# Optimization experiments

Hardware: AMD Instinct MI355X
Metric: run time of the kernel (lower is better)

## Reference

```python
import jax, jax.numpy as jnp
import numpy as np

B, S, D, DQK, DV = 4, 2048, 1024, 128, 256
EPS = 1e-8


def setup_inputs() -> dict:
    key = jax.random.key(0)
    ks = jax.random.split(key, 11)
    s = lambda fan_in: 1.0 / np.sqrt(fan_in)
    return {
        "X": jax.random.normal(ks[0], (B, S, D), dtype=jnp.float32),
        "Wq": jax.random.uniform(ks[1], (D, DQK), minval=-s(D), maxval=s(D), dtype=jnp.float32),
        "bq": jax.random.uniform(ks[2], (DQK,), minval=-s(D), maxval=s(D), dtype=jnp.float32),
        "Wk": jax.random.uniform(ks[3], (D, DQK), minval=-s(D), maxval=s(D), dtype=jnp.float32),
        "bk": jax.random.uniform(ks[4], (DQK,), minval=-s(D), maxval=s(D), dtype=jnp.float32),
        "Wv": jax.random.uniform(ks[5], (D, DV), minval=-s(D), maxval=s(D), dtype=jnp.float32),
        "bv": jax.random.uniform(ks[6], (DV,), minval=-s(D), maxval=s(D), dtype=jnp.float32),
        "Wg": jax.random.uniform(ks[7], (D, DV), minval=-s(D), maxval=s(D), dtype=jnp.float32),
        "bg": jax.random.uniform(ks[8], (DV,), minval=-s(D), maxval=s(D), dtype=jnp.float32),
        "Wp": jax.random.uniform(ks[9], (DV, D), minval=-s(DV), maxval=s(DV), dtype=jnp.float32),
        "bp": jax.random.uniform(ks[10], (D,), minval=-s(DV), maxval=s(DV), dtype=jnp.float32),
    }


def _shepards(Q, K, V, p=2, eps=EPS):
    # Euclidean cdist via ||q||^2 + ||k||^2 - 2 q.k  (then sqrt)
    q2 = jnp.sum(Q * Q, axis=-1, keepdims=True)          # [B,Sq,1]
    k2 = jnp.sum(K * K, axis=-1, keepdims=True)          # [B,Sk,1]
    d2 = q2 + jnp.swapaxes(k2, -1, -2) - 2.0 * jnp.einsum("bqd,bkd->bqk", Q, K)
    Dm = jnp.sqrt(jnp.maximum(d2, 0.0))                  # [B,Sq,Sk]
    W = jnp.power(jnp.maximum(Dm, eps), -float(p))
    A = W / jnp.sum(W, axis=2, keepdims=True)
    return jnp.einsum("bqk,bkv->bqv", A, V)


def reference(X, Wq, bq, Wk, bk, Wv, bv, Wg, bg, Wp, bp):
    N = X  # norm is Identity
    Q = N @ Wq + bq
    K = N @ Wk + bk
    V = N @ Wv + bv
    A = _shepards(Q, K, V)
    G = N @ Wg + bg
    return X + (A * G) @ Wp + bp
```

## Files before the change

### kernel.cpp

```cpp
#include <hip/hip_runtime.h>
#include <stdint.h>

#define SLEN 2048
#define NROWS 8192

typedef __attribute__((ext_vector_type(4))) float f32x4;
typedef __attribute__((ext_vector_type(8))) short bf16x8;
typedef __attribute__((ext_vector_type(2))) unsigned int u32x2;
typedef __attribute__((ext_vector_type(4))) unsigned int u32x4;

__device__ __forceinline__ short f2bf(float f) {
  uint32_t u = __builtin_bit_cast(uint32_t, f);
  u += 0x7FFFu + ((u >> 16) & 1u);
  return (short)(u >> 16);
}
__device__ __forceinline__ float bf2f(short s) {
  uint32_t u = ((uint32_t)(uint16_t)s) << 16;
  return __builtin_bit_cast(float, u);
}
__device__ __forceinline__ f32x4 mfma16(bf16x8 a, bf16x8 b, f32x4 c) {
  return __builtin_amdgcn_mfma_f32_16x16x32_bf16(a, b, c, 0, 0, 0);
}
__device__ __forceinline__ void gld_lds16(const void* g, void* l) {
  __builtin_amdgcn_global_load_lds(
      (const __attribute__((address_space(1))) void*)g,
      (__attribute__((address_space(3))) void*)l, 16, 0, 0);
}

__global__ __launch_bounds__(256) void k_prep(
    const float* __restrict__ Wq, const float* __restrict__ bq,
    const float* __restrict__ Wk, const float* __restrict__ bk,
    const float* __restrict__ Wv, const float* __restrict__ bv,
    const float* __restrict__ Wg, const float* __restrict__ bg,
    const float* __restrict__ Wp,
    short* __restrict__ WcatT, short* __restrict__ WpT,
    float* __restrict__ bcat) {
  __shared__ short tl[64][72];
  int blk = blockIdx.x, tid = threadIdx.x;
  if (blk < 256) {
    int t = blk;
    const float* src; short* dst; int C, rowoff, dstC, r0, c0;
    if (t < 32)       { src = Wq; C = 128;  rowoff = 0;   dst = WcatT; dstC = 1024; r0 = (t >> 1) * 64;  c0 = (t & 1) * 64; }
    else if (t < 64)  { t -= 32;  src = Wk; C = 128;  rowoff = 128; dst = WcatT; dstC = 1024; r0 = (t >> 1) * 64;  c0 = (t & 1) * 64; }
    else if (t < 128) { t -= 64;  src = Wv; C = 256;  rowoff = 256; dst = WcatT; dstC = 1024; r0 = (t >> 2) * 64;  c0 = (t & 3) * 64; }
    else if (t < 192) { t -= 128; src = Wg; C = 256;  rowoff = 512; dst = WcatT; dstC = 1024; r0 = (t >> 2) * 64;  c0 = (t & 3) * 64; }
    else              { t -= 192; src = Wp; C = 1024; rowoff = 0;   dst = WpT;   dstC = 256;  r0 = (t >> 4) * 64;  c0 = (t & 15) * 64; }
    int lr = tid >> 4, lcc = tid & 15;
#pragma unroll
    for (int rr = 0; rr < 4; ++rr) {
      f32x4 v = *(const f32x4*)&src[(size_t)(r0 + lr * 4 + rr) * C + c0 + lcc * 4];
#pragma unroll
      for (int j = 0; j < 4; ++j) tl[lcc * 4 + j][lr * 4 + rr] = f2bf(v[j]);
    }
    __syncthreads();
    int orow = tid >> 2, og = (tid & 3) * 16;
    bf16x8 o1, o2;
#pragma unroll
    for (int j = 0; j < 8; ++j) { o1[j] = tl[orow][og + j]; o2[j] = tl[orow][og + 8 + j]; }
    size_t dbase = (size_t)(rowoff + c0 + orow) * dstC + r0 + og;
    *(bf16x8*)&dst[dbase] = o1;
    *(bf16x8*)&dst[dbase + 8] = o2;
  } else {
    int c = tid;
    if (c < 768) {
      float v;
      if (c < 128)      v = bq[c];
      else if (c < 256) v = bk[c - 128];
      else if (c < 512) v = bv[c - 256];
      else              v = bg[c - 512];
      bcat[c] = v;
    }
  }
}

__global__ __launch_bounds__(256) void k_gemm1(
    const float* __restrict__ X, const short* __restrict__ WcatT,
    const float* __restrict__ bcat, short* __restrict__ O,
    float* __restrict__ q2a, float* __restrict__ k2a) {
  __shared__ float Atf[128 * 32];
  __shared__ short Bt[128 * 32];
  __shared__ float nlds[128][2];
  const int tid = threadIdx.x;
  const int w = tid >> 6, l = tid & 63, lg = l >> 4, lc = l & 15;
  const int m0 = blockIdx.x * 128, n0 = blockIdx.y * 128;
  const int sr0 = w * 32 + (l >> 2);
  const int scc = (l & 3) * 8;
  const int wm = (w >> 1) * 64, wn = (w & 1) * 64;
  const int arow = w * 8 + (l >> 3);
  const int achk = (l & 7) ^ (arow & 7);

  f32x4 acc[4][4] = {};
  const float* Ab = X + (size_t)m0 * 1024;
  const short* Bb = WcatT + (size_t)n0 * 1024;

  for (int kb = 0; kb < 1024; kb += 32) {
#pragma unroll
    for (int i = 0; i < 4; ++i)
      gld_lds16(Ab + (size_t)(i * 32 + arow) * 1024 + kb + achk * 4,
                &Atf[(i * 32 + w * 8) * 32 + l * 4]);
    gld_lds16(Bb + (size_t)sr0 * 1024 + kb + scc, &Bt[(w * 32) * 32]);
    gld_lds16(Bb + (size_t)(sr0 + 16) * 1024 + kb + scc, &Bt[(w * 32 + 16) * 32]);
    __syncthreads();
    bf16x8 af[4], bf[4];
#pragma unroll
    for (int mi = 0; mi < 4; ++mi) {
      int r = wm + mi * 16 + lc;
      f32x4 a0 = *(const f32x4*)&Atf[r * 32 + (((2 * lg) ^ (r & 7)) * 4)];
      f32x4 a1 = *(const f32x4*)&Atf[r * 32 + (((2 * lg + 1) ^ (r & 7)) * 4)];
#pragma unroll
      for (int j = 0; j < 4; ++j) {
        af[mi][j] = f2bf(a0[j]);
        af[mi][4 + j] = f2bf(a1[j]);
      }
    }
#pragma unroll
    for (int ni = 0; ni < 4; ++ni)
      bf[ni] = *(const bf16x8*)&Bt[(wn + ni * 16 + lc) * 32 + lg * 8];
#pragma unroll
    for (int mi = 0; mi < 4; ++mi)
#pragma unroll
      for (int ni = 0; ni < 4; ++ni)
        acc[mi][ni] = mfma16(af[mi], bf[ni], acc[mi][ni]);
    __syncthreads();
  }
  float sq[4][4] = {};
#pragma unroll
  for (int mi = 0; mi < 4; ++mi) {
    int gr = m0 + wm + mi * 16 + lg * 4;
#pragma unroll
    for (int ni = 0; ni < 4; ++ni) {
      int gc = n0 + wn + ni * 16 + lc;
      float bias = bcat[gc];
#pragma unroll
      for (int r = 0; r < 4; ++r) {
        short sv = f2bf(acc[mi][ni][r] + bias);
        O[(size_t)(gr + r) * 768 + gc] = sv;
        float v = bf2f(sv);
        sq[mi][r] += v * v;
      }
    }
  }
  if (blockIdx.y < 2) {
#pragma unroll
    for (int mi = 0; mi < 4; ++mi)
#pragma unroll
      for (int r = 0; r < 4; ++r) {
        float v = sq[mi][r];
        v += __shfl_xor(v, 1, 64); v += __shfl_xor(v, 2, 64);
        v += __shfl_xor(v, 4, 64); v += __shfl_xor(v, 8, 64);
        sq[mi][r] = v;
      }
    if (lc == 0) {
#pragma unroll
      for (int mi = 0; mi < 4; ++mi)
#pragma unroll
        for (int r = 0; r < 4; ++r)
          nlds[wm + mi * 16 + lg * 4 + r][w & 1] = sq[mi][r];
    }
    __syncthreads();
    if (tid < 128) {
      float t = nlds[tid][0] + nlds[tid][1];
      (blockIdx.y == 0 ? q2a : k2a)[m0 + tid] = t;
    }
  }
}

__global__ __launch_bounds__(256) void k_vt(
    const short* __restrict__ O, short* __restrict__ Vtp) {
  __shared__ short tile[64][33];
  int blk = blockIdx.x, tid = threadIdx.x;
  int b = blk >> 8, rem = blk & 255;
  int s0 = (rem >> 3) * 64, dv0 = (rem & 7) * 32;
  int r = tid >> 2, cg = (tid & 3) * 8;
  bf16x8 v = *(const bf16x8*)&O[(size_t)(b * SLEN + s0 + r) * 768 + 256 + dv0 + cg];
#pragma unroll
  for (int j = 0; j < 8; ++j) tile[r][cg + j] = v[j];
  __syncthreads();
  int dr = tid >> 3, sg = (tid & 7) * 8;
  bf16x8 ov;
#pragma unroll
  for (int j = 0; j < 8; ++j) ov[j] = tile[sg + j][dr];
  int ka = s0 + sg;
  int c5 = ka >> 5, hi = (ka >> 4) & 1, lgq = (ka >> 2) & 3;
  size_t base = (size_t)(b * 256 + dv0 + dr) * SLEN + c5 * 32 + lgq * 8 + hi * 4;
  u32x4 od = __builtin_bit_cast(u32x4, ov);
  u32x2 p0; p0[0] = od[0]; p0[1] = od[1];
  u32x2 p1; p1[0] = od[2]; p1[1] = od[3];
  *(u32x2*)&Vtp[base] = p0;
  *(u32x2*)&Vtp[base + 8] = p1;
}

__global__ __launch_bounds__(512) void k_attn(
    const short* __restrict__ O, const short* __restrict__ Vtp,
    const float* __restrict__ q2a, const float* __restrict__ k2a,
    short* __restrict__ nump, float* __restrict__ denp) {
  __shared__ short Klds[2][64 * 128];
  __shared__ short Vlds[2][256 * 64];
  const int tid = threadIdx.x;
  const int w = tid >> 6, l = tid & 63, lg = l >> 4, lc = l & 15;
  const int gid = blockIdx.x;
  const int blk = ((gid & 7) << 5) | (gid >> 3);
  const int b = blk >> 6, qt = (blk >> 2) & 15, ks = blk & 3;
  const int grow0 = b * SLEN + qt * 128 + w * 16;
  const int kbase = ks * 512;

  bf16x8 qf[4];
#pragma unroll
  for (int kf = 0; kf < 4; ++kf)
    qf[kf] = *(const bf16x8*)&O[(size_t)(grow0 + lc) * 768 + kf * 32 + lg * 8];
  const float q2s = q2a[grow0 + lc];

  f32x4 acc[16] = {};
  float den = 0.f;

#define STAGE(T, BSEL)                                                        \
  {                                                                           \
    const int kt_ = kbase + (T) * 64;                                         \
    _Pragma("unroll")                                                         \
    for (int j = 0; j < 6; ++j) {                                             \
      int issue = w * 6 + j;                                                  \
      if (issue < 16) {                                                       \
        int kk = issue * 4 + (l >> 4);                                        \
        int c = l & 15;                                                       \
        const short* src = O + (size_t)(b * SLEN + kt_ + kk) * 768 + 128 +    \
                           ((c ^ (kk & 7)) * 8);                              \
        gld_lds16(src, &Klds[BSEL][issue * 512 + l * 8]);                     \
      } else {                                                                \
        int vj = issue - 16;                                                  \
        int dv = vj * 8 + (l >> 3);                                           \
        int c = l & 7;                                                        \
        const short* src = Vtp + (size_t)(b * 256 + dv) * SLEN + kt_ +        \
                           ((c ^ (dv & 7)) * 8);                              \
        gld_lds16(src, &Vlds[BSEL][vj * 512 + l * 8]);                        \
      }                                                                       \
    }                                                                         \
  }

  STAGE(0, 0);
  for (int t = 0; t < 8; ++t) {
    __syncthreads();
    if (t < 7) STAGE(t + 1, (t + 1) & 1);
    const int bsel = t & 1;
    const int kb = b * SLEN + kbase + t * 64;
    f32x4 s[4] = {};
#pragma unroll
    for (int e = 0; e < 4; ++e)
#pragma unroll
      for (int kf = 0; kf < 4; ++kf) {
        bf16x8 kv = *(const bf16x8*)&Klds[bsel][(e * 16 + lc) * 128 +
                                               (((kf * 4 + lg) ^ (lc & 7)) * 8)];
        s[e] = mfma16(kv, qf[kf], s[e]);
      }
    float wv[4][4];
#pragma unroll
    for (int e = 0; e < 4; ++e) {
      f32x4 k2v = *(const f32x4*)&k2a[kb + e * 16 + lg * 4];
#pragma unroll
      for (int r = 0; r < 4; ++r) {
        float d2 = q2s + k2v[r] - 2.0f * s[e][r];
        float g = __builtin_amdgcn_rcpf(fmaxf(d2, 1e-16f));
        wv[e][r] = g;
        den += g;
      }
    }
#pragma unroll
    for (int ksub = 0; ksub < 2; ++ksub) {
      bf16x8 pa;
#pragma unroll
      for (int r = 0; r < 4; ++r) {
        pa[r] = f2bf(wv[2 * ksub][r]);
        pa[4 + r] = f2bf(wv[2 * ksub + 1][r]);
      }
#pragma unroll
      for (int nv = 0; nv < 16; ++nv) {
        int dv = nv * 16 + lc;
        bf16x8 bv = *(const bf16x8*)&Vlds[bsel][dv * 64 +
                                               (((ksub * 4 + lg) ^ (dv & 7)) * 8)];
        acc[nv] = mfma16(pa, bv, acc[nv]);
      }
    }
  }
#undef STAGE
  den += __shfl_xor(den, 16, 64);
  den += __shfl_xor(den, 32, 64);
  const int qt32 = qt * 4 + (w >> 1);
  const int pb = ((b * 64 + qt32) << 2) | ks;
  if (l < 16) denp[pb * 32 + (w & 1) * 16 + lc] = den;
  const size_t pbase = (size_t)pb * 32 * 256;
#pragma unroll
  for (int nv = 0; nv < 16; ++nv) {
    int dv = nv * 16 + lc;
#pragma unroll
    for (int r = 0; r < 4; ++r) {
      int rit = (w & 1) * 16 + lg * 4 + r;
      nump[pbase + (size_t)rit * 256 + dv] = f2bf(acc[nv][r]);
    }
  }
}

__global__ __launch_bounds__(256) void k_gemm3(
    const short* __restrict__ nump, const float* __restrict__ denp,
    const short* __restrict__ O, const short* __restrict__ WpT,
    const float* __restrict__ X, const float* __restrict__ bp,
    float* __restrict__ Y) {
  __shared__ short AGt[128 * 256];
  __shared__ short Bt[128 * 32];
  const int tid = threadIdx.x;
  const int w = tid >> 6, l = tid & 63, lg = l >> 4, lc = l & 15;
  const int bid = blockIdx.x;
  const int m0 = (bid & 63) * 128, n0 = (bid >> 6) * 128;
  const int sr0 = w * 32 + (l >> 2);
  const int scc = (l & 3) * 8;
  const int wm = (w >> 1) * 64, wn = (w & 1) * 64;

  {
    int r = tid >> 1;
    int row = m0 + r;
    int b_ = row >> 11, srow = row & 2047;
    int qt = srow >> 5, rit = srow & 31;
    int pbb = (b_ * 64 + qt) * 4;
    float den = 0.f;
#pragma unroll
    for (int ksi = 0; ksi < 4; ++ksi) den += denp[(pbb + ksi) * 32 + rit];
    float rden = 1.f / den;
    int dvh = (tid & 1) * 128;
#pragma unroll
    for (int ch = 0; ch < 16; ++ch) {
      int dv0 = dvh + ch * 8;
      float num[8] = {};
#pragma unroll
      for (int ksi = 0; ksi < 4; ++ksi) {
        bf16x8 v = *(const bf16x8*)&nump[((size_t)(pbb + ksi) * 32 + rit) * 256 + dv0];
#pragma unroll
        for (int j = 0; j < 8; ++j) num[j] += bf2f(v[j]);
      }
      bf16x8 gv = *(const bf16x8*)&O[(size_t)row * 768 + 512 + dv0];
      bf16x8 o;
#pragma unroll
      for (int j = 0; j < 8; ++j) o[j] = f2bf(num[j] * rden * bf2f(gv[j]));
      int byte = (r * 512 + dv0 * 2) ^ ((r & 31) << 4);
      *(bf16x8*)((char*)AGt + byte) = o;
    }
  }

  f32x4 acc[4][4] = {};
  const short* Bb = WpT + (size_t)n0 * 256;

  for (int kb = 0; kb < 256; kb += 32) {
    gld_lds16(Bb + (size_t)sr0 * 256 + kb + scc, &Bt[(w * 32) * 32]);
    gld_lds16(Bb + (size_t)(sr0 + 16) * 256 + kb + scc, &Bt[(w * 32 + 16) * 32]);
    __syncthreads();
    bf16x8 af[4], bf[4];
#pragma unroll
    for (int mi = 0; mi < 4; ++mi) {
      int r = wm + mi * 16 + lc;
      int byte = (r * 512 + (kb + lg * 8) * 2) ^ ((r & 31) << 4);
      af[mi] = *(const bf16x8*)((const char*)AGt + byte);
    }
#pragma unroll
    for (int ni = 0; ni < 4; ++ni)
      bf[ni] = *(const bf16x8*)&Bt[(wn + ni * 16 + lc) * 32 + lg * 8];
#pragma unroll
    for (int mi = 0; mi < 4; ++mi)
#pragma unroll
      for (int ni = 0; ni < 4; ++ni)
        acc[mi][ni] = mfma16(af[mi], bf[ni], acc[mi][ni]);
    __syncthreads();
  }
#pragma unroll
  for (int mi = 0; mi < 4; ++mi) {
    int gr = m0 + wm + mi * 16 + lg * 4;
#pragma unroll
    for (int ni = 0; ni < 4; ++ni) {
      int gc = n0 + wn + ni * 16 + lc;
      float bias = bp[gc];
#pragma unroll
      for (int r = 0; r < 4; ++r) {
        size_t idx = (size_t)(gr + r) * 1024 + gc;
        Y[idx] = acc[mi][ni][r] + X[idx] + bias;
      }
    }
  }
}

extern "C" void kernel_launch(void* const* d_in, const int* in_sizes, int n_in,
                              void* d_out, int out_size, void* d_ws, size_t ws_size,
                              hipStream_t stream) {
  const float* X  = (const float*)d_in[0];
  const float* Wq = (const float*)d_in[1];
  const float* bq = (const float*)d_in[2];
  const float* Wk = (const float*)d_in[3];
  const float* bk = (const float*)d_in[4];
  const float* Wv = (const float*)d_in[5];
  const float* bv = (const float*)d_in[6];
  const float* Wg = (const float*)d_in[7];
  const float* bg = (const float*)d_in[8];
  const float* Wp = (const float*)d_in[9];
  const float* bp = (const float*)d_in[10];

  char* ws = (char*)d_ws;
  short* WcatT = (short*)(ws + 0);
  short* WpT   = (short*)(ws + 1572864);
  float* bcat  = (float*)(ws + 2097152);
  short* O     = (short*)(ws + 2101248);
  short* Vtp   = (short*)(ws + 14684160);
  float* q2a   = (float*)(ws + 18878464);
  float* k2a   = (float*)(ws + 18911232);
  short* nump  = (short*)(ws + 18944000);
  float* denp  = (float*)(ws + 35721216);
  float* Y = (float*)d_out;

  hipLaunchKernelGGL(k_prep, dim3(257), dim3(256), 0, stream,
                     Wq, bq, Wk, bk, Wv, bv, Wg, bg, Wp, WcatT, WpT, bcat);
  hipLaunchKernelGGL(k_gemm1, dim3(64, 6), dim3(256), 0, stream, X, WcatT, bcat, O, q2a, k2a);
  hipLaunchKernelGGL(k_vt, dim3(1024), dim3(256), 0, stream, O, Vtp);
  hipLaunchKernelGGL(k_attn, dim3(256), dim3(512), 0, stream, O, Vtp, q2a, k2a, nump, denp);
  hipLaunchKernelGGL(k_gemm3, dim3(512), dim3(256), 0, stream, nump, denp, O, WpT, X, bp, Y);
}
```

Baseline: 216.8 us.

## Split split-K reduction and gating out of output GEMM into separate kernel

Moves the reduction of the partial numerators and denominators, the normalisation and the gate multiply out of k_gemm3 into a new elementwise kernel k_red that writes a bf16 AG buffer. k_gemm3 then becomes a plain tiled GEMM that streams both A and B through small LDS tiles instead of a 64KB LDS A panel. Before, each of the 8 column blocks redundantly recomputed the reduction for its rows. The aim is to remove that redundant work and raise occupancy, at the cost of one extra launch and an extra write and read of AG.

```diff
diff --git a/kernel.cpp b/kernel.cpp
--- a/kernel.cpp
+++ b/kernel.cpp
@@ -298,65 +298,61 @@
   }
 }
 
+__global__ __launch_bounds__(256) void k_red(
+    const short* __restrict__ nump, const float* __restrict__ denp,
+    const short* __restrict__ O, short* __restrict__ AG) {
+  int flat = blockIdx.x * 256 + threadIdx.x;
+  int idx8 = flat * 8;
+  int row = idx8 >> 8;
+  int dv0 = idx8 & 255;
+  int b = row >> 11, srow = row & 2047;
+  int qt = srow >> 5, rit = srow & 31;
+  int blkbase = (b * 64 + qt) << 2;
+  float num[8] = {};
+  float den = 0.f;
+#pragma unroll
+  for (int ksi = 0; ksi < 4; ++ksi) {
+    const size_t base = ((size_t)(blkbase + ksi) * 32 + rit) * 256 + dv0;
+    bf16x8 v = *(const bf16x8*)&nump[base];
+#pragma unroll
+    for (int j = 0; j < 8; ++j) num[j] += bf2f(v[j]);
+    den += denp[(blkbase + ksi) * 32 + rit];
+  }
+  float rden = 1.f / den;
+  bf16x8 gv = *(const bf16x8*)&O[(size_t)row * 768 + 512 + dv0];
+  bf16x8 o;
+#pragma unroll
+  for (int j = 0; j < 8; ++j) o[j] = f2bf(num[j] * rden * bf2f(gv[j]));
+  *(bf16x8*)&AG[idx8] = o;
+}
+
 __global__ __launch_bounds__(256) void k_gemm3(
-    const short* __restrict__ nump, const float* __restrict__ denp,
-    const short* __restrict__ O, const short* __restrict__ WpT,
+    const short* __restrict__ AG, const short* __restrict__ WpT,
     const float* __restrict__ X, const float* __restrict__ bp,
     float* __restrict__ Y) {
-  __shared__ short AGt[128 * 256];
+  __shared__ short At[128 * 32];
   __shared__ short Bt[128 * 32];
   const int tid = threadIdx.x;
   const int w = tid >> 6, l = tid & 63, lg = l >> 4, lc = l & 15;
-  const int bid = blockIdx.x;
-  const int m0 = (bid & 63) * 128, n0 = (bid >> 6) * 128;
+  const int m0 = blockIdx.x * 128, n0 = blockIdx.y * 128;
   const int sr0 = w * 32 + (l >> 2);
   const int scc = (l & 3) * 8;
   const int wm = (w >> 1) * 64, wn = (w & 1) * 64;
 
-  {
-    int r = tid >> 1;
-    int row = m0 + r;
-    int b_ = row >> 11, srow = row & 2047;
-    int qt = srow >> 5, rit = srow & 31;
-    int pbb = (b_ * 64 + qt) * 4;
-    float den = 0.f;
-#pragma unroll
-    for (int ksi = 0; ksi < 4; ++ksi) den += denp[(pbb + ksi) * 32 + rit];
-    float rden = 1.f / den;
-    int dvh = (tid & 1) * 128;
-#pragma unroll
-    for (int ch = 0; ch < 16; ++ch) {
-      int dv0 = dvh + ch * 8;
-      float num[8] = {};
-#pragma unroll
-      for (int ksi = 0; ksi < 4; ++ksi) {
-        bf16x8 v = *(const bf16x8*)&nump[((size_t)(pbb + ksi) * 32 + rit) * 256 + dv0];
-#pragma unroll
-        for (int j = 0; j < 8; ++j) num[j] += bf2f(v[j]);
-      }
-      bf16x8 gv = *(const bf16x8*)&O[(size_t)row * 768 + 512 + dv0];
-      bf16x8 o;
-#pragma unroll
-      for (int j = 0; j < 8; ++j) o[j] = f2bf(num[j] * rden * bf2f(gv[j]));
-      int byte = (r * 512 + dv0 * 2) ^ ((r & 31) << 4);
-      *(bf16x8*)((char*)AGt + byte) = o;
-    }
-  }
-
   f32x4 acc[4][4] = {};
+  const short* Ab = AG + (size_t)m0 * 256;
   const short* Bb = WpT + (size_t)n0 * 256;
 
   for (int kb = 0; kb < 256; kb += 32) {
+    gld_lds16(Ab + (size_t)sr0 * 256 + kb + scc, &At[(w * 32) * 32]);
+    gld_lds16(Ab + (size_t)(sr0 + 16) * 256 + kb + scc, &At[(w * 32 + 16) * 32]);
     gld_lds16(Bb + (size_t)sr0 * 256 + kb + scc, &Bt[(w * 32) * 32]);
     gld_lds16(Bb + (size_t)(sr0 + 16) * 256 + kb + scc, &Bt[(w * 32 + 16) * 32]);
     __syncthreads();
     bf16x8 af[4], bf[4];
 #pragma unroll
-    for (int mi = 0; mi < 4; ++mi) {
-      int r = wm + mi * 16 + lc;
-      int byte = (r * 512 + (kb + lg * 8) * 2) ^ ((r & 31) << 4);
-      af[mi] = *(const bf16x8*)((const char*)AGt + byte);
-    }
+    for (int mi = 0; mi < 4; ++mi)
+      af[mi] = *(const bf16x8*)&At[(wm + mi * 16 + lc) * 32 + lg * 8];
 #pragma unroll
     for (int ni = 0; ni < 4; ++ni)
       bf[ni] = *(const bf16x8*)&Bt[(wn + ni * 16 + lc) * 32 + lg * 8];
@@ -408,6 +404,7 @@
   float* k2a   = (float*)(ws + 18911232);
   short* nump  = (short*)(ws + 18944000);
   float* denp  = (float*)(ws + 35721216);
+  short* AG    = (short*)(ws + 35852288);
   float* Y = (float*)d_out;
 
   hipLaunchKernelGGL(k_prep, dim3(257), dim3(256), 0, stream,
@@ -415,5 +412,6 @@
   hipLaunchKernelGGL(k_gemm1, dim3(64, 6), dim3(256), 0, stream, X, WcatT, bcat, O, q2a, k2a);
   hipLaunchKernelGGL(k_vt, dim3(1024), dim3(256), 0, stream, O, Vtp);
   hipLaunchKernelGGL(k_attn, dim3(256), dim3(512), 0, stream, O, Vtp, q2a, k2a, nump, denp);
-  hipLaunchKernelGGL(k_gemm3, dim3(512), dim3(256), 0, stream, nump, denp, O, WpT, X, bp, Y);
-}
+  hipLaunchKernelGGL(k_red, dim3(1024), dim3(256), 0, stream, nump, denp, O, AG);
+  hipLaunchKernelGGL(k_gemm3, dim3(64, 8), dim3(256), 0, stream, AG, WpT, X, bp, Y);
+}
```

New measurement: 194.9 us. -10.1%, faster.
